# Performance work log

Hardware: AMD Instinct MI355X
Metric: run time of the kernel (lower is better)

## Reference

```python
import jax, jax.numpy as jnp
import numpy as np

B, N, M, D, H = 4, 1024, 1024, 1024, 16
HD = D // H
MH = int(D * 4.0 * 2 / 3)  # SwiGLU hidden = 2730
EPS = 1e-6


def setup_inputs() -> dict:
    key = jax.random.key(0)
    ks = jax.random.split(key, 16)
    w = lambda k, shape: jax.random.normal(k, shape, jnp.float32) * 0.02
    return dict(
        x=jax.random.normal(ks[0], (B, N, D), jnp.float32),
        source_tokens=jax.random.normal(ks[1], (B, M, D), jnp.float32),
        c=jax.random.normal(ks[2], (B, D), jnp.float32),
        ada_w=w(ks[3], (D, 9 * D)), ada_b=jnp.zeros((9 * D,), jnp.float32),
        n1_w=jnp.ones((D,), jnp.float32), nc_w=jnp.ones((D,), jnp.float32), n2_w=jnp.ones((D,), jnp.float32),
        sa_qkv_w=w(ks[4], (D, 3 * D)), sa_qkv_b=jnp.zeros((3 * D,), jnp.float32),
        sa_qn_w=jnp.ones((HD,), jnp.float32), sa_kn_w=jnp.ones((HD,), jnp.float32),
        sa_o_w=w(ks[5], (D, D)), sa_o_b=jnp.zeros((D,), jnp.float32),
        ca_q_w=w(ks[6], (D, D)), ca_q_b=jnp.zeros((D,), jnp.float32),
        ca_kv_w=w(ks[7], (D, 2 * D)), ca_kv_b=jnp.zeros((2 * D,), jnp.float32),
        ca_qn_w=jnp.ones((HD,), jnp.float32), ca_kn_w=jnp.ones((HD,), jnp.float32),
        ca_o_w=w(ks[8], (D, D)), ca_o_b=jnp.zeros((D,), jnp.float32),
        mlp_w1=w(ks[9], (D, MH)), mlp_b1=jnp.zeros((MH,), jnp.float32),
        mlp_w2=w(ks[10], (D, MH)), mlp_b2=jnp.zeros((MH,), jnp.float32),
        mlp_w3=w(ks[11], (MH, D)), mlp_b3=jnp.zeros((D,), jnp.float32),
    )


def _rms(x, w):
    return x * jax.lax.rsqrt(jnp.mean(x * x, axis=-1, keepdims=True) + EPS) * w


def _modulate(x, shift, scale):
    return x * (1.0 + scale[:, None, :]) + shift[:, None, :]


def _sdpa(q, k, v):
    # q: (B,Nq,H,HD), k/v: (B,Nk,H,HD)
    s = jnp.einsum('bqhd,bkhd->bhqk', q, k) * (HD ** -0.5)
    a = jax.nn.softmax(s, axis=-1)
    o = jnp.einsum('bhqk,bkhd->bqhd', a, v)
    return o.reshape(q.shape[0], q.shape[1], D)


def reference(x, source_tokens, c, ada_w, ada_b, n1_w, nc_w, n2_w,
              sa_qkv_w, sa_qkv_b, sa_qn_w, sa_kn_w, sa_o_w, sa_o_b,
              ca_q_w, ca_q_b, ca_kv_w, ca_kv_b, ca_qn_w, ca_kn_w, ca_o_w, ca_o_b,
              mlp_w1, mlp_b1, mlp_w2, mlp_b2, mlp_w3, mlp_b3):
    mods = jax.nn.silu(c) @ ada_w + ada_b
    (shift_sa, scale_sa, gate_sa, shift_ca, scale_ca, gate_ca,
     shift_ff, scale_ff, gate_ff) = jnp.split(mods, 9, axis=-1)

    # --- self-attention sublayer ---
    xn = _modulate(_rms(x, n1_w), shift_sa, scale_sa)
    qkv = xn @ sa_qkv_w + sa_qkv_b
    q, k, v = jnp.split(qkv, 3, axis=-1)
    q = _rms(q.reshape(B, N, H, HD), sa_qn_w)
    k = _rms(k.reshape(B, N, H, HD), sa_kn_w)
    v = v.reshape(B, N, H, HD)
    attn = _sdpa(q, k, v) @ sa_o_w + sa_o_b
    x = x + gate_sa[:, None, :] * attn

    # --- cross-attention sublayer ---
    xn = _modulate(_rms(x, nc_w), shift_ca, scale_ca)
    q = (xn @ ca_q_w + ca_q_b).reshape(B, N, H, HD)
    kv = source_tokens @ ca_kv_w + ca_kv_b
    k, v = jnp.split(kv, 2, axis=-1)
    q = _rms(q, ca_qn_w)
    k = _rms(k.reshape(B, M, H, HD), ca_kn_w)
    v = v.reshape(B, M, H, HD)
    cattn = _sdpa(q, k, v) @ ca_o_w + ca_o_b
    x = x + gate_ca[:, None, :] * cattn

    # --- SwiGLU FFN sublayer ---
    xn = _modulate(_rms(x, n2_w), shift_ff, scale_ff)
    ff = (jax.nn.silu(xn @ mlp_w1 + mlp_b1) * (xn @ mlp_w2 + mlp_b2)) @ mlp_w3 + mlp_b3
    x = x + gate_ff[:, None, :] * ff
    return x
```

## Files before the change

kernel.cpp:

```cpp
#include <hip/hip_runtime.h>

typedef unsigned short u16;
typedef __attribute__((ext_vector_type(8))) short short8;
typedef __attribute__((ext_vector_type(4))) float f32x4;

#define DD 1024
#define NN 1024
#define MODS_LD 9216

__device__ __forceinline__ float bf2f(u16 v) {
  unsigned int u = ((unsigned int)v) << 16;
  return __builtin_bit_cast(float, u);
}
__device__ __forceinline__ u16 f2bf(float f) {
  unsigned int u = __builtin_bit_cast(unsigned int, f);
  unsigned int lsb = (u >> 16) & 1;
  u += 0x7fffu + lsb;
  return (u16)(u >> 16);
}
__device__ __forceinline__ unsigned cvtpk_bf16(float a, float b) {
  unsigned r;
  asm volatile("v_cvt_pk_bf16_f32 %0, %1, %2" : "=v"(r) : "v"(a), "v"(b));
  return r;
}

__device__ __forceinline__ void gload_lds16(const u16* g, u16* l) {
  __builtin_amdgcn_global_load_lds(
      (const __attribute__((address_space(1))) unsigned int*)g,
      (__attribute__((address_space(3))) unsigned int*)l, 16, 0, 0);
}

__device__ __forceinline__ void xcd_tile(int ncolChunks, int cr, int cc, int& tm, int& tn) {
  int id = blockIdx.x;
  int c = id & 7, i = id >> 3;
  int chunkRow = c / ncolChunks, chunkCol = c % ncolChunks;
  tm = chunkRow * cr + (i % cr);
  tn = chunkCol * cc + (i / cr);
}

__global__ void transpose_convert(const float* __restrict__ src, u16* __restrict__ dst,
                                  int R, int C, int R2, int C2) {
  __shared__ float tile[32][33];
  int tx = threadIdx.x, ty = threadIdx.y;
  int r0 = blockIdx.x * 32, c0 = blockIdx.y * 32;
#pragma unroll
  for (int i = 0; i < 4; ++i) {
    int r = r0 + ty + i * 8, c = c0 + tx;
    tile[ty + i * 8][tx] = (r < R && c < C) ? src[(long)r * C + c] : 0.f;
  }
  __syncthreads();
#pragma unroll
  for (int i = 0; i < 4; ++i) {
    int c = c0 + ty + i * 8, r = r0 + tx;
    if (c < C2 && r < R2) dst[(long)c * R2 + r] = f2bf(tile[tx][ty + i * 8]);
  }
}

__global__ void cvt_bf16_kernel(const float* __restrict__ in, u16* __restrict__ out, long n4) {
  long i = (long)blockIdx.x * 256 + threadIdx.x;
  if (i >= n4) return;
  float4 v = *(const float4*)&in[i * 4];
  ushort4 pk = {f2bf(v.x), f2bf(v.y), f2bf(v.z), f2bf(v.w)};
  *(ushort4*)&out[i * 4] = pk;
}

__global__ void silu_kernel(const float* __restrict__ c, float* __restrict__ sc) {
  int i = blockIdx.x * 256 + threadIdx.x;
  float v = c[i];
  sc[i] = v / (1.f + __expf(-v));
}

#define MODS_KS 32
__global__ __launch_bounds__(256) void mods_partial(const float* __restrict__ sc,
                                                    const float* __restrict__ aw,
                                                    float* __restrict__ part) {
  int j = blockIdx.x * 256 + threadIdx.x;
  int ks = blockIdx.y;
  int d0 = ks * (DD / MODS_KS);
  float a0 = 0.f, a1 = 0.f, a2 = 0.f, a3 = 0.f;
#pragma unroll 8
  for (int d = d0; d < d0 + DD / MODS_KS; ++d) {
    float w = aw[(long)d * MODS_LD + j];
    a0 = fmaf(sc[d], w, a0);
    a1 = fmaf(sc[DD + d], w, a1);
    a2 = fmaf(sc[2 * DD + d], w, a2);
    a3 = fmaf(sc[3 * DD + d], w, a3);
  }
  long base = (long)ks * 4 * MODS_LD + j;
  part[base] = a0;
  part[base + MODS_LD] = a1;
  part[base + 2 * MODS_LD] = a2;
  part[base + 3 * MODS_LD] = a3;
}

__global__ __launch_bounds__(256) void mods_reduce(const float* __restrict__ part,
                                                   const float* __restrict__ ab,
                                                   float* __restrict__ mods) {
  int j = blockIdx.x * 256 + threadIdx.x;
  int b = blockIdx.y;
  float acc = ab[j];
#pragma unroll
  for (int ks = 0; ks < MODS_KS; ++ks) acc += part[((long)ks * 4 + b) * MODS_LD + j];
  mods[(long)b * MODS_LD + j] = acc;
}

__global__ __launch_bounds__(256) void rmsmod_kernel(const float* __restrict__ x,
                                                     const float* __restrict__ w,
                                                     const float* __restrict__ mods,
                                                     int shiftOff, int scaleOff,
                                                     u16* __restrict__ out) {
  long row = blockIdx.x;
  int b = (int)(row >> 10);
  int t = threadIdx.x;
  const float* xr = x + row * DD;
  float4 v = *(const float4*)&xr[t * 4];
  float ss = v.x * v.x + v.y * v.y + v.z * v.z + v.w * v.w;
#pragma unroll
  for (int msk = 1; msk < 64; msk <<= 1) ss += __shfl_xor(ss, msk);
  __shared__ float red[4];
  if ((t & 63) == 0) red[t >> 6] = ss;
  __syncthreads();
  float tot = red[0] + red[1] + red[2] + red[3];
  float inv = rsqrtf(tot * (1.f / DD) + 1e-6f);
  const float* mrow = mods + (long)b * MODS_LD;
  float vv[4] = {v.x, v.y, v.z, v.w};
  u16 tmp[4];
#pragma unroll
  for (int j = 0; j < 4; ++j) {
    int c = t * 4 + j;
    float rr = vv[j] * inv * w[c] * (1.f + mrow[scaleOff + c]) + mrow[shiftOff + c];
    tmp[j] = f2bf(rr);
  }
  ushort4 pk = {tmp[0], tmp[1], tmp[2], tmp[3]};
  *(ushort4*)&out[row * DD + t * 4] = pk;
}

__global__ void vtrans_kernel(const u16* __restrict__ vb, int kvStride, int Mpb,
                              u16* __restrict__ vt) {
  __shared__ u16 tile[64][66];
  int t = threadIdx.x;
  int kt = blockIdx.x, h = blockIdx.y, b = blockIdx.z;
  const u16* base = vb + ((long)(b * Mpb + kt * 64)) * kvStride + h * 64;
#pragma unroll
  for (int sh = 0; sh < 2; ++sh) {
    int r = sh * 32 + (t >> 3);
    int c0 = (t & 7) * 8;
    short8 vv = *(const short8*)(base + (long)r * kvStride + c0);
#pragma unroll
    for (int j = 0; j < 8; ++j) tile[c0 + j][r] = (u16)vv[j];
  }
  __syncthreads();
  u16* obase = vt + ((long)(b * 16 + h) * 64) * 1024 + kt * 64;
#pragma unroll
  for (int sh = 0; sh < 2; ++sh) {
    int d = sh * 32 + (t >> 3);
    int c0 = (t & 7) * 8;
    u16 tmp[8];
#pragma unroll
    for (int j = 0; j < 8; ++j) tmp[j] = tile[d][c0 + j];
    *(short8*)(obase + (long)d * 1024 + c0) = *(short8*)tmp;
  }
}

template <int MODE, int BN, int MINW, int NORM>
__global__ __launch_bounds__(256, MINW) void gemm_bf16(
    const u16* __restrict__ A, const u16* __restrict__ Bt, int K, int ldc,
    const float* __restrict__ bias, int biasN, u16* __restrict__ outb,
    float* __restrict__ outf, const float* __restrict__ xin,
    const float* __restrict__ mods, int gateOff, int ncolChunks, int cr, int cc,
    const float* __restrict__ nw, int normLo, int normHi, float nscale) {
  constexpr int WC = BN / 2;
  constexpr int NT = WC / 16;
  constexpr int LOADS = 4 + BN / 32;
  __shared__ u16 As[2][128 * 64];
  __shared__ u16 Bs[2][BN * 64];
  int t = threadIdx.x;
  int l = t & 63, w = t >> 6;
  int wr = w >> 1, wc = w & 1;
  int lg = l >> 4, ll = l & 15;
  int rx = ll & 7;
  int tm, tn;
  xcd_tile(ncolChunks, cr, cc, tm, tn);
  long rowTile = (long)tm * 128;
  long colTile = (long)tn * BN;
  const u16* Ap = A + rowTile * K;
  const u16* Bp = Bt + colTile * K;
  int srow = t >> 3;
  int sck = ((t & 7) ^ (srow & 7)) * 8;

  auto stage = [&](int buf, int k0) {
#pragma unroll
    for (int i = 0; i < 4; ++i)
      gload_lds16(Ap + (long)(i * 32 + srow) * K + k0 + sck, &As[buf][(i * 256 + t) * 8]);
#pragma unroll
    for (int i = 0; i < BN / 32; ++i)
      gload_lds16(Bp + (long)(i * 32 + srow) * K + k0 + sck, &Bs[buf][(i * 256 + t) * 8]);
  };

  const int ntk = K >> 6;
  stage(0, 0);
  if (ntk > 1) stage(1, 64);

  f32x4 acc[4][NT] = {};
  int cur = 0;
  for (int i = 0; i < ntk; ++i) {
    if (i + 1 < ntk) {
      asm volatile("s_waitcnt vmcnt(%0)" ::"i"(LOADS) : "memory");
    } else {
      asm volatile("s_waitcnt vmcnt(0)" ::: "memory");
    }
    __builtin_amdgcn_s_barrier();
    const u16* Ac = As[cur];
    const u16* Bc = Bs[cur];
    short8 af[2][4], bfr[2][NT];
#pragma unroll
    for (int kk = 0; kk < 2; ++kk) {
#pragma unroll
      for (int m2 = 0; m2 < 4; ++m2)
        af[kk][m2] =
            *(const short8*)&Ac[(wr * 64 + m2 * 16 + ll) * 64 + (((kk * 4 + lg) ^ rx) << 3)];
#pragma unroll
      for (int n2 = 0; n2 < NT; ++n2)
        bfr[kk][n2] =
            *(const short8*)&Bc[(wc * WC + n2 * 16 + ll) * 64 + (((kk * 4 + lg) ^ rx) << 3)];
    }
    asm volatile("s_waitcnt lgkmcnt(0)" ::: "memory");
    __builtin_amdgcn_sched_barrier(0);
    __builtin_amdgcn_s_barrier();
    if (i + 2 < ntk) stage(cur, (i + 2) * 64);
    __builtin_amdgcn_s_setprio(1);
#pragma unroll
    for (int kk = 0; kk < 2; ++kk)
#pragma unroll
      for (int m2 = 0; m2 < 4; ++m2)
#pragma unroll
        for (int n2 = 0; n2 < NT; ++n2)
          acc[m2][n2] = __builtin_amdgcn_mfma_f32_16x16x32_bf16(af[kk][m2], bfr[kk][n2],
                                                                acc[m2][n2], 0, 0, 0);
    __builtin_amdgcn_s_setprio(0);
    cur ^= 1;
  }

  if (NORM == 1 && tn >= normLo && tn < normHi) {
    float bv[NT], wnv[NT];
#pragma unroll
    for (int n2 = 0; n2 < NT; ++n2) {
      long cg = colTile + wc * WC + n2 * 16 + ll;
      bv[n2] = bias[cg];
      wnv[n2] = nw[n2 * 16 + ll];
    }
#pragma unroll
    for (int m2 = 0; m2 < 4; ++m2) {
#pragma unroll
      for (int r = 0; r < 4; ++r) {
        float vals[NT];
        float ss = 0.f;
#pragma unroll
        for (int n2 = 0; n2 < NT; ++n2) {
          vals[n2] = acc[m2][n2][r] + bv[n2];
          ss += vals[n2] * vals[n2];
        }
        ss += __shfl_xor(ss, 1);
        ss += __shfl_xor(ss, 2);
        ss += __shfl_xor(ss, 4);
        ss += __shfl_xor(ss, 8);
        float inv = rsqrtf(ss * (1.f / 64) + 1e-6f) * nscale;
        long rg = rowTile + wr * 64 + m2 * 16 + lg * 4 + r;
#pragma unroll
        for (int n2 = 0; n2 < NT; ++n2) {
          long cg = colTile + wc * WC + n2 * 16 + ll;
          outb[rg * ldc + cg] = f2bf(vals[n2] * inv * wnv[n2]);
        }
      }
    }
    return;
  }

#pragma unroll
  for (int n2 = 0; n2 < NT; ++n2) {
    long cg = colTile + wc * WC + n2 * 16 + ll;
    float bv = (cg < biasN) ? bias[cg] : 0.f;
#pragma unroll
    for (int m2 = 0; m2 < 4; ++m2) {
#pragma unroll
      for (int r = 0; r < 4; ++r) {
        long rg = rowTile + wr * 64 + m2 * 16 + lg * 4 + r;
        float v = acc[m2][n2][r] + bv;
        long idx = rg * ldc + cg;
        if (MODE == 0) {
          outb[idx] = f2bf(v);
        } else {
          int bb = (int)(rg >> 10);
          outf[idx] = xin[idx] + mods[(long)bb * MODS_LD + gateOff + cg] * v;
        }
      }
    }
  }
}

__global__ __launch_bounds__(256, 2) void gemm_dual_swiglu(
    const u16* __restrict__ A, const u16* __restrict__ B1t, const u16* __restrict__ B2t,
    int K, int ldc, const float* __restrict__ b1, const float* __restrict__ b2, int biasN,
    u16* __restrict__ outb, int ncolChunks, int cr, int cc) {
  constexpr int BN = 64, WC = 32, NT = 2;
  __shared__ u16 As[2][128 * 64];
  __shared__ u16 B1s[2][BN * 64];
  __shared__ u16 B2s[2][BN * 64];
  int t = threadIdx.x;
  int l = t & 63, w = t >> 6;
  int wr = w >> 1, wc = w & 1;
  int lg = l >> 4, ll = l & 15;
  int rx = ll & 7;
  int tm, tn;
  xcd_tile(ncolChunks, cr, cc, tm, tn);
  long rowTile = (long)tm * 128;
  long colTile = (long)tn * BN;
  const u16* Ap = A + rowTile * K;
  const u16* B1p = B1t + colTile * K;
  const u16* B2p = B2t + colTile * K;
  int srow = t >> 3;
  int sck = ((t & 7) ^ (srow & 7)) * 8;

  auto stage = [&](int buf, int k0) {
#pragma unroll
    for (int i = 0; i < 4; ++i)
      gload_lds16(Ap + (long)(i * 32 + srow) * K + k0 + sck, &As[buf][(i * 256 + t) * 8]);
#pragma unroll
    for (int i = 0; i < 2; ++i) {
      gload_lds16(B1p + (long)(i * 32 + srow) * K + k0 + sck, &B1s[buf][(i * 256 + t) * 8]);
      gload_lds16(B2p + (long)(i * 32 + srow) * K + k0 + sck, &B2s[buf][(i * 256 + t) * 8]);
    }
  };

  const int ntk = K >> 6;
  stage(0, 0);
  if (ntk > 1) stage(1, 64);

  f32x4 acc1[4][NT] = {}, acc2[4][NT] = {};
  int cur = 0;
  for (int i = 0; i < ntk; ++i) {
    if (i + 1 < ntk) {
      asm volatile("s_waitcnt vmcnt(8)" ::: "memory");
    } else {
      asm volatile("s_waitcnt vmcnt(0)" ::: "memory");
    }
    __builtin_amdgcn_s_barrier();
    const u16* Ac = As[cur];
    const u16* B1c = B1s[cur];
    const u16* B2c = B2s[cur];
    short8 af[2][4], b1f[2][NT], b2f[2][NT];
#pragma unroll
    for (int kk = 0; kk < 2; ++kk) {
#pragma unroll
      for (int m2 = 0; m2 < 4; ++m2)
        af[kk][m2] =
            *(const short8*)&Ac[(wr * 64 + m2 * 16 + ll) * 64 + (((kk * 4 + lg) ^ rx) << 3)];
#pragma unroll
      for (int n2 = 0; n2 < NT; ++n2) {
        int off = (wc * WC + n2 * 16 + ll) * 64 + (((kk * 4 + lg) ^ rx) << 3);
        b1f[kk][n2] = *(const short8*)&B1c[off];
        b2f[kk][n2] = *(const short8*)&B2c[off];
      }
    }
    asm volatile("s_waitcnt lgkmcnt(0)" ::: "memory");
    __builtin_amdgcn_sched_barrier(0);
    __builtin_amdgcn_s_barrier();
    if (i + 2 < ntk) stage(cur, (i + 2) * 64);
    __builtin_amdgcn_s_setprio(1);
#pragma unroll
    for (int kk = 0; kk < 2; ++kk)
#pragma unroll
      for (int m2 = 0; m2 < 4; ++m2)
#pragma unroll
        for (int n2 = 0; n2 < NT; ++n2) {
          acc1[m2][n2] = __builtin_amdgcn_mfma_f32_16x16x32_bf16(af[kk][m2], b1f[kk][n2],
                                                                 acc1[m2][n2], 0, 0, 0);
          acc2[m2][n2] = __builtin_amdgcn_mfma_f32_16x16x32_bf16(af[kk][m2], b2f[kk][n2],
                                                                 acc2[m2][n2], 0, 0, 0);
        }
    __builtin_amdgcn_s_setprio(0);
    cur ^= 1;
  }
#pragma unroll
  for (int n2 = 0; n2 < NT; ++n2) {
    long cg = colTile + wc * WC + n2 * 16 + ll;
    float bv1 = (cg < biasN) ? b1[cg] : 0.f;
    float bv2 = (cg < biasN) ? b2[cg] : 0.f;
#pragma unroll
    for (int m2 = 0; m2 < 4; ++m2) {
#pragma unroll
      for (int r = 0; r < 4; ++r) {
        long rg = rowTile + wr * 64 + m2 * 16 + lg * 4 + r;
        float v1 = acc1[m2][n2][r] + bv1;
        float v2 = acc2[m2][n2][r] + bv2;
        float sg = v1 / (1.f + __expf(-v1));
        outb[rg * ldc + cg] = f2bf(sg * v2);
      }
    }
  }
}

__global__ __launch_bounds__(256, 3) void attn_kernel(
    const u16* __restrict__ qb, int qStride, const u16* __restrict__ kb, int kvStride,
    const u16* __restrict__ vt, const float* __restrict__ qn, u16* __restrict__ outp,
    int Nk, int Mpb) {
  __shared__ u16 Qs[64 * 64];
  __shared__ u16 Ks[2][64 * 64];
  __shared__ u16 Vs[2][64 * 64];
  __shared__ u16 Ps[4][16 * 64];
  int t = threadIdx.x, w = t >> 6, l = t & 63;
  int h = blockIdx.x, b = blockIdx.y, qt = blockIdx.z;
  int lg = l >> 4, ll = l & 15;
  int rx = ll & 7;

  const u16* Qbase = qb + ((long)(b * NN + qt * 64)) * qStride + h * 64;
  const u16* Kbase = kb + ((long)b * Mpb) * kvStride + h * 64;
  const u16* Vbase = vt + ((long)(b * 16 + h) * 64) * 1024;

  int srow = t >> 3;
  int schunk = t & 7;

#pragma unroll
  for (int sh = 0; sh < 2; ++sh) {
    int row = sh * 32 + srow;
    int ck = schunk ^ (row & 7);
    gload_lds16(Qbase + (long)row * qStride + ck * 8, &Qs[sh * 2048 + t * 8]);
  }
  auto stageKV = [&](int buf, int kt) {
    const u16* kn = Kbase + (long)kt * 64 * kvStride;
    const u16* vn = Vbase + kt * 64;
#pragma unroll
    for (int sh = 0; sh < 2; ++sh) {
      int row = sh * 32 + srow;
      int ck = schunk ^ (row & 7);
      gload_lds16(kn + (long)row * kvStride + ck * 8, &Ks[buf][sh * 2048 + t * 8]);
      gload_lds16(vn + (long)row * 1024 + ck * 8, &Vs[buf][sh * 2048 + t * 8]);
    }
  };
  const int ntk = Nk >> 6;
  stageKV(0, 0);
  if (ntk > 1) stageKV(1, 1);

  short8 qf0, qf1;
  float mrun = -1e30f, ssum = 0.f;
  f32x4 o[4] = {};

  int cur = 0;
  for (int kt = 0; kt < ntk; ++kt) {
    if (kt + 1 < ntk) {
      asm volatile("s_waitcnt vmcnt(4)" ::: "memory");
    } else {
      asm volatile("s_waitcnt vmcnt(0)" ::: "memory");
    }
    __builtin_amdgcn_s_barrier();
    if (kt == 0) {
      qf0 = *(const short8*)&Qs[(w * 16 + ll) * 64 + ((lg ^ rx) << 3)];
      qf1 = *(const short8*)&Qs[(w * 16 + ll) * 64 + (((4 + lg) ^ rx) << 3)];
      float qv0[8], qv1[8], ss = 0.f;
#pragma unroll
      for (int j = 0; j < 8; ++j) {
        qv0[j] = bf2f((u16)qf0[j]);
        qv1[j] = bf2f((u16)qf1[j]);
        ss += qv0[j] * qv0[j] + qv1[j] * qv1[j];
      }
      ss += __shfl_xor(ss, 16);
      ss += __shfl_xor(ss, 32);
      float inv = rsqrtf(ss * (1.f / 64) + 1e-6f) * 0.125f;
      int d0 = (lg ^ rx) << 3, d1 = ((4 + lg) ^ rx) << 3;
      u16 t0[8], t1[8];
#pragma unroll
      for (int j = 0; j < 8; ++j) {
        t0[j] = f2bf(qv0[j] * inv * qn[d0 + j]);
        t1[j] = f2bf(qv1[j] * inv * qn[d1 + j]);
      }
      qf0 = *(short8*)t0;
      qf1 = *(short8*)t1;
    }
    const u16* Kc = Ks[cur];
    f32x4 s[4] = {};
#pragma unroll
    for (int n = 0; n < 4; ++n) {
      short8 kf0 = *(const short8*)&Kc[(n * 16 + ll) * 64 + ((lg ^ rx) << 3)];
      short8 kf1 = *(const short8*)&Kc[(n * 16 + ll) * 64 + (((4 + lg) ^ rx) << 3)];
      s[n] = __builtin_amdgcn_mfma_f32_16x16x32_bf16(kf0, qf0, s[n], 0, 0, 0);
      s[n] = __builtin_amdgcn_mfma_f32_16x16x32_bf16(kf1, qf1, s[n], 0, 0, 0);
    }
    float t0 = fmaxf(fmaxf(s[0][0], s[0][1]), fmaxf(s[0][2], s[0][3]));
    float t1 = fmaxf(fmaxf(s[1][0], s[1][1]), fmaxf(s[1][2], s[1][3]));
    float t2 = fmaxf(fmaxf(s[2][0], s[2][1]), fmaxf(s[2][2], s[2][3]));
    float t3 = fmaxf(fmaxf(s[3][0], s[3][1]), fmaxf(s[3][2], s[3][3]));
    float pm = fmaxf(fmaxf(t0, t1), fmaxf(t2, t3));
    pm = fmaxf(pm, __shfl_xor(pm, 16));
    pm = fmaxf(pm, __shfl_xor(pm, 32));
    float nm = fmaxf(mrun, pm);
    float alpha = __expf(mrun - nm);
    float pn[4][4];
#pragma unroll
    for (int n = 0; n < 4; ++n)
#pragma unroll
      for (int r = 0; r < 4; ++r) pn[n][r] = __expf(s[n][r] - nm);
    float r0 = (pn[0][0] + pn[0][1]) + (pn[0][2] + pn[0][3]);
    float r1 = (pn[1][0] + pn[1][1]) + (pn[1][2] + pn[1][3]);
    float r2 = (pn[2][0] + pn[2][1]) + (pn[2][2] + pn[2][3]);
    float r3 = (pn[3][0] + pn[3][1]) + (pn[3][2] + pn[3][3]);
    float rs = (r0 + r1) + (r2 + r3);
    rs += __shfl_xor(rs, 16);
    rs += __shfl_xor(rs, 32);
    ssum = ssum * alpha + rs;
    mrun = nm;
#pragma unroll
    for (int n = 0; n < 4; ++n) {
      uint2 pkd;
      pkd.x = cvtpk_bf16(pn[n][0], pn[n][1]);
      pkd.y = cvtpk_bf16(pn[n][2], pn[n][3]);
      int gran = n * 2 + (lg >> 1);
      int perm = gran ^ rx;
      *(uint2*)&Ps[w][ll * 64 + perm * 8 + (lg & 1) * 4] = pkd;
    }
    float a0 = __shfl(alpha, lg * 4 + 0);
    float a1 = __shfl(alpha, lg * 4 + 1);
    float a2 = __shfl(alpha, lg * 4 + 2);
    float a3 = __shfl(alpha, lg * 4 + 3);
#pragma unroll
    for (int n = 0; n < 4; ++n) {
      o[n][0] *= a0;
      o[n][1] *= a1;
      o[n][2] *= a2;
      o[n][3] *= a3;
    }
    short8 pf0 = *(const short8*)&Ps[w][ll * 64 + ((lg ^ rx) << 3)];
    short8 pf1 = *(const short8*)&Ps[w][ll * 64 + (((4 + lg) ^ rx) << 3)];
    const u16* Vc = Vs[cur];
    short8 vfr[4][2];
#pragma unroll
    for (int n = 0; n < 4; ++n) {
      vfr[n][0] = *(const short8*)&Vc[(n * 16 + ll) * 64 + ((lg ^ rx) << 3)];
      vfr[n][1] = *(const short8*)&Vc[(n * 16 + ll) * 64 + (((4 + lg) ^ rx) << 3)];
    }
    asm volatile("s_waitcnt lgkmcnt(0)" ::: "memory");
    __builtin_amdgcn_sched_barrier(0);
    __builtin_amdgcn_s_barrier();
    if (kt + 2 < ntk) stageKV(cur, kt + 2);
    __builtin_amdgcn_s_setprio(1);
#pragma unroll
    for (int n = 0; n < 4; ++n) {
      o[n] = __builtin_amdgcn_mfma_f32_16x16x32_bf16(pf0, vfr[n][0], o[n], 0, 0, 0);
      o[n] = __builtin_amdgcn_mfma_f32_16x16x32_bf16(pf1, vfr[n][1], o[n], 0, 0, 0);
    }
    __builtin_amdgcn_s_setprio(0);
    cur ^= 1;
  }
  float s0 = __shfl(ssum, lg * 4 + 0);
  float s1 = __shfl(ssum, lg * 4 + 1);
  float s2 = __shfl(ssum, lg * 4 + 2);
  float s3 = __shfl(ssum, lg * 4 + 3);
  float i0 = 1.f / s0, i1 = 1.f / s1, i2 = 1.f / s2, i3 = 1.f / s3;
#pragma unroll
  for (int n = 0; n < 4; ++n) {
    float ir[4] = {i0, i1, i2, i3};
#pragma unroll
    for (int r = 0; r < 4; ++r) {
      long row = (long)b * NN + qt * 64 + w * 16 + lg * 4 + r;
      int col = h * 64 + n * 16 + ll;
      outp[row * DD + col] = f2bf(o[n][r] * ir[r]);
    }
  }
}

extern "C" void kernel_launch(void* const* d_in, const int* in_sizes, int n_in,
                              void* d_out, int out_size, void* d_ws, size_t ws_size,
                              hipStream_t stream) {
  const float* x = (const float*)d_in[0];
  const float* src = (const float*)d_in[1];
  const float* c = (const float*)d_in[2];
  const float* ada_w = (const float*)d_in[3];
  const float* ada_b = (const float*)d_in[4];
  const float* n1_w = (const float*)d_in[5];
  const float* nc_w = (const float*)d_in[6];
  const float* n2_w = (const float*)d_in[7];
  const float* sa_qkv_w = (const float*)d_in[8];
  const float* sa_qkv_b = (const float*)d_in[9];
  const float* sa_qn_w = (const float*)d_in[10];
  const float* sa_kn_w = (const float*)d_in[11];
  const float* sa_o_w = (const float*)d_in[12];
  const float* sa_o_b = (const float*)d_in[13];
  const float* ca_q_w = (const float*)d_in[14];
  const float* ca_q_b = (const float*)d_in[15];
  const float* ca_kv_w = (const float*)d_in[16];
  const float* ca_kv_b = (const float*)d_in[17];
  const float* ca_qn_w = (const float*)d_in[18];
  const float* ca_kn_w = (const float*)d_in[19];
  const float* ca_o_w = (const float*)d_in[20];
  const float* ca_o_b = (const float*)d_in[21];
  const float* mlp_w1 = (const float*)d_in[22];
  const float* mlp_b1 = (const float*)d_in[23];
  const float* mlp_w2 = (const float*)d_in[24];
  const float* mlp_b2 = (const float*)d_in[25];
  const float* mlp_w3 = (const float*)d_in[26];
  const float* mlp_b3 = (const float*)d_in[27];
  float* out = (float*)d_out;

  char* p = (char*)d_ws;
  auto alloc = [&](size_t bytes) {
    char* r = p;
    p += (bytes + 255) & ~(size_t)255;
    return r;
  };
  float* mods = (float*)alloc(4l * 9216 * 4);
  float* sc = (float*)alloc(4096l * 4);
  float* part = (float*)alloc((long)MODS_KS * 4 * 9216 * 4);
  u16* qkvT = (u16*)alloc(3072l * 1024 * 2);
  u16* saoT = (u16*)alloc(1024l * 1024 * 2);
  u16* caqT = (u16*)alloc(1024l * 1024 * 2);
  u16* cakvT = (u16*)alloc(2048l * 1024 * 2);
  u16* caoT = (u16*)alloc(1024l * 1024 * 2);
  u16* w1T = (u16*)alloc(2816l * 1024 * 2);
  u16* w2T = (u16*)alloc(2816l * 1024 * 2);
  u16* w3T = (u16*)alloc(1024l * 2816 * 2);
  u16* xnb = (u16*)alloc(4096l * 1024 * 2);
  u16* srcb = (u16*)alloc(4096l * 1024 * 2);
  u16* bufA = (u16*)alloc(4096l * 3072 * 2);
  u16* bufB = (u16*)alloc(4096l * 2816 * 2);
  u16* attO = (u16*)alloc(4096l * 1024 * 2);
  u16* vtb = xnb;

  dim3 tb(32, 8);
  transpose_convert<<<dim3(32, 96), tb, 0, stream>>>(sa_qkv_w, qkvT, 1024, 3072, 1024, 3072);
  transpose_convert<<<dim3(32, 32), tb, 0, stream>>>(sa_o_w, saoT, 1024, 1024, 1024, 1024);
  transpose_convert<<<dim3(32, 32), tb, 0, stream>>>(ca_q_w, caqT, 1024, 1024, 1024, 1024);
  transpose_convert<<<dim3(32, 64), tb, 0, stream>>>(ca_kv_w, cakvT, 1024, 2048, 1024, 2048);
  transpose_convert<<<dim3(32, 32), tb, 0, stream>>>(ca_o_w, caoT, 1024, 1024, 1024, 1024);
  transpose_convert<<<dim3(32, 88), tb, 0, stream>>>(mlp_w1, w1T, 1024, 2730, 1024, 2816);
  transpose_convert<<<dim3(32, 88), tb, 0, stream>>>(mlp_w2, w2T, 1024, 2730, 1024, 2816);
  transpose_convert<<<dim3(88, 32), tb, 0, stream>>>(mlp_w3, w3T, 2730, 1024, 2816, 1024);
  cvt_bf16_kernel<<<4096, 256, 0, stream>>>(src, srcb, 4096l * 1024 / 4);
  silu_kernel<<<16, 256, 0, stream>>>(c, sc);
  mods_partial<<<dim3(36, MODS_KS), 256, 0, stream>>>(sc, ada_w, part);
  mods_reduce<<<dim3(36, 4), 256, 0, stream>>>(part, ada_b, mods);

  rmsmod_kernel<<<4096, 256, 0, stream>>>(x, n1_w, mods, 0, 1024, xnb);
  gemm_bf16<0, 128, 2, 1><<<768, 256, 0, stream>>>(xnb, qkvT, 1024, 3072, sa_qkv_b, 3072, bufA,
                                                   nullptr, nullptr, nullptr, 0, 4, 16, 6,
                                                   sa_kn_w, 8, 16, 1.0f);
  vtrans_kernel<<<dim3(16, 16, 4), 256, 0, stream>>>(bufA + 2048, 3072, 1024, vtb);
  attn_kernel<<<dim3(16, 4, 16), 256, 0, stream>>>(bufA, 3072, bufA + 1024, 3072, vtb, sa_qn_w,
                                                   attO, 1024, 1024);
  gemm_bf16<1, 64, 3, 0><<<512, 256, 0, stream>>>(attO, saoT, 1024, 1024, sa_o_b, 1024, nullptr,
                                                  out, x, mods, 2048, 2, 8, 8, nullptr, 0, 0,
                                                  0.f);

  rmsmod_kernel<<<4096, 256, 0, stream>>>(out, nc_w, mods, 3072, 4096, xnb);
  gemm_bf16<0, 64, 3, 0><<<512, 256, 0, stream>>>(xnb, caqT, 1024, 1024, ca_q_b, 1024, bufA,
                                                  nullptr, nullptr, nullptr, 0, 2, 8, 8,
                                                  nullptr, 0, 0, 0.f);
  gemm_bf16<0, 128, 2, 1><<<512, 256, 0, stream>>>(srcb, cakvT, 1024, 2048, ca_kv_b, 2048, bufB,
                                                   nullptr, nullptr, nullptr, 0, 2, 8, 8,
                                                   ca_kn_w, 0, 8, 1.0f);
  vtrans_kernel<<<dim3(16, 16, 4), 256, 0, stream>>>(bufB + 1024, 2048, 1024, vtb);
  attn_kernel<<<dim3(16, 4, 16), 256, 0, stream>>>(bufA, 1024, bufB, 2048, vtb, ca_qn_w, attO,
                                                   1024, 1024);
  gemm_bf16<1, 64, 3, 0><<<512, 256, 0, stream>>>(attO, caoT, 1024, 1024, ca_o_b, 1024, nullptr,
                                                  out, out, mods, 5120, 2, 8, 8, nullptr, 0, 0,
                                                  0.f);

  rmsmod_kernel<<<4096, 256, 0, stream>>>(out, n2_w, mods, 6144, 7168, xnb);
  gemm_dual_swiglu<<<1408, 256, 0, stream>>>(xnb, w1T, w2T, 1024, 2816, mlp_b1, mlp_b2, 2730,
                                             bufA, 4, 16, 11);
  gemm_bf16<1, 64, 3, 0><<<512, 256, 0, stream>>>(bufA, w3T, 2816, 1024, mlp_b3, 1024, nullptr,
                                                  out, out, mods, 8192, 2, 8, 8, nullptr, 0, 0,
                                                  0.f);
}
```

Measured before the change: 372.2 us.

## Batch weight transposes, fuse SiLU into mods, use lazy-rescale exp2 softmax

Eight separate weight transpose launches become one launch that reads a table of descriptors. The SiLU kernel is folded into mods_partial through a small shared-memory staging step. The attention softmax now works in base 2: log2(e) is folded into the Q scale and v_exp_f32 is called directly. The running max is only updated, and the output only rescaled, when the new block max exceeds the old one by more than 8, which cuts exp and multiply work per tile at the cost of a small added overflow and precision risk.

Measured after the change: 362.3 us. 2.7% less time.

```diff
diff --git a/kernel.cpp b/kernel.cpp
--- a/kernel.cpp
+++ b/kernel.cpp
@@ -21,6 +21,11 @@
 __device__ __forceinline__ unsigned cvtpk_bf16(float a, float b) {
   unsigned r;
   asm volatile("v_cvt_pk_bf16_f32 %0, %1, %2" : "=v"(r) : "v"(a), "v"(b));
+  return r;
+}
+__device__ __forceinline__ float exp2x(float x) {
+  float r;
+  asm("v_exp_f32 %0, %1" : "=v"(r) : "v"(x));
   return r;
 }
 
@@ -38,11 +43,29 @@
   tn = chunkCol * cc + (i / cr);
 }
 
-__global__ void transpose_convert(const float* __restrict__ src, u16* __restrict__ dst,
-                                  int R, int C, int R2, int C2) {
+struct TDesc {
+  const float* s;
+  u16* d;
+  int R, C, R2, C2, gx, start;
+};
+struct TPack {
+  TDesc t[8];
+};
+
+__global__ void transpose_all(TPack p) {
   __shared__ float tile[32][33];
+  int id = blockIdx.x;
+  int k = 0;
+#pragma unroll
+  for (int j = 1; j < 8; ++j)
+    if (id >= p.t[j].start) k = j;
+  const float* src = p.t[k].s;
+  u16* dst = p.t[k].d;
+  int R = p.t[k].R, C = p.t[k].C, R2 = p.t[k].R2, C2 = p.t[k].C2;
+  int rem = id - p.t[k].start;
+  int gx = p.t[k].gx;
+  int r0 = (rem % gx) * 32, c0 = (rem / gx) * 32;
   int tx = threadIdx.x, ty = threadIdx.y;
-  int r0 = blockIdx.x * 32, c0 = blockIdx.y * 32;
 #pragma unroll
   for (int i = 0; i < 4; ++i) {
     int r = r0 + ty + i * 8, c = c0 + tx;
@@ -64,27 +87,31 @@
   *(ushort4*)&out[i * 4] = pk;
 }
 
-__global__ void silu_kernel(const float* __restrict__ c, float* __restrict__ sc) {
-  int i = blockIdx.x * 256 + threadIdx.x;
-  float v = c[i];
-  sc[i] = v / (1.f + __expf(-v));
-}
-
 #define MODS_KS 32
-__global__ __launch_bounds__(256) void mods_partial(const float* __restrict__ sc,
+__global__ __launch_bounds__(256) void mods_partial(const float* __restrict__ c,
                                                     const float* __restrict__ aw,
                                                     float* __restrict__ part) {
+  __shared__ float scs[4][32];
   int j = blockIdx.x * 256 + threadIdx.x;
   int ks = blockIdx.y;
   int d0 = ks * (DD / MODS_KS);
+  int t = threadIdx.x;
+  if (t < 32) {
+#pragma unroll
+    for (int b2 = 0; b2 < 4; ++b2) {
+      float v = c[b2 * DD + d0 + t];
+      scs[b2][t] = v / (1.f + __expf(-v));
+    }
+  }
+  __syncthreads();
   float a0 = 0.f, a1 = 0.f, a2 = 0.f, a3 = 0.f;
 #pragma unroll 8
-  for (int d = d0; d < d0 + DD / MODS_KS; ++d) {
-    float w = aw[(long)d * MODS_LD + j];
-    a0 = fmaf(sc[d], w, a0);
-    a1 = fmaf(sc[DD + d], w, a1);
-    a2 = fmaf(sc[2 * DD + d], w, a2);
-    a3 = fmaf(sc[3 * DD + d], w, a3);
+  for (int d = 0; d < DD / MODS_KS; ++d) {
+    float w = aw[(long)(d0 + d) * MODS_LD + j];
+    a0 = fmaf(scs[0][d], w, a0);
+    a1 = fmaf(scs[1][d], w, a1);
+    a2 = fmaf(scs[2][d], w, a2);
+    a3 = fmaf(scs[3][d], w, a3);
   }
   long base = (long)ks * 4 * MODS_LD + j;
   part[base] = a0;
@@ -465,7 +492,7 @@
       }
       ss += __shfl_xor(ss, 16);
       ss += __shfl_xor(ss, 32);
-      float inv = rsqrtf(ss * (1.f / 64) + 1e-6f) * 0.125f;
+      float inv = rsqrtf(ss * (1.f / 64) + 1e-6f) * (0.125f * 1.44269504f);
       int d0 = (lg ^ rx) << 3, d1 = ((4 + lg) ^ rx) << 3;
       u16 t0[8], t1[8];
 #pragma unroll
@@ -492,13 +519,13 @@
     float pm = fmaxf(fmaxf(t0, t1), fmaxf(t2, t3));
     pm = fmaxf(pm, __shfl_xor(pm, 16));
     pm = fmaxf(pm, __shfl_xor(pm, 32));
-    float nm = fmaxf(mrun, pm);
-    float alpha = __expf(mrun - nm);
+    bool resc = !__all(pm - mrun <= 8.f);
+    float nm = resc ? fmaxf(mrun, pm) : mrun;
     float pn[4][4];
 #pragma unroll
     for (int n = 0; n < 4; ++n)
 #pragma unroll
-      for (int r = 0; r < 4; ++r) pn[n][r] = __expf(s[n][r] - nm);
+      for (int r = 0; r < 4; ++r) pn[n][r] = exp2x(s[n][r] - nm);
     float r0 = (pn[0][0] + pn[0][1]) + (pn[0][2] + pn[0][3]);
     float r1 = (pn[1][0] + pn[1][1]) + (pn[1][2] + pn[1][3]);
     float r2 = (pn[2][0] + pn[2][1]) + (pn[2][2] + pn[2][3]);
@@ -506,7 +533,23 @@
     float rs = (r0 + r1) + (r2 + r3);
     rs += __shfl_xor(rs, 16);
     rs += __shfl_xor(rs, 32);
-    ssum = ssum * alpha + rs;
+    if (resc) {
+      float alpha = exp2x(mrun - nm);
+      ssum = ssum * alpha + rs;
+      float a0 = __shfl(alpha, lg * 4 + 0);
+      float a1 = __shfl(alpha, lg * 4 + 1);
+      float a2 = __shfl(alpha, lg * 4 + 2);
+      float a3 = __shfl(alpha, lg * 4 + 3);
+#pragma unroll
+      for (int n = 0; n < 4; ++n) {
+        o[n][0] *= a0;
+        o[n][1] *= a1;
+        o[n][2] *= a2;
+        o[n][3] *= a3;
+      }
+    } else {
+      ssum += rs;
+    }
     mrun = nm;
 #pragma unroll
     for (int n = 0; n < 4; ++n) {
@@ -516,17 +559,6 @@
       int gran = n * 2 + (lg >> 1);
       int perm = gran ^ rx;
       *(uint2*)&Ps[w][ll * 64 + perm * 8 + (lg & 1) * 4] = pkd;
-    }
-    float a0 = __shfl(alpha, lg * 4 + 0);
-    float a1 = __shfl(alpha, lg * 4 + 1);
-    float a2 = __shfl(alpha, lg * 4 + 2);
-    float a3 = __shfl(alpha, lg * 4 + 3);
-#pragma unroll
-    for (int n = 0; n < 4; ++n) {
-      o[n][0] *= a0;
-      o[n][1] *= a1;
-      o[n][2] *= a2;
-      o[n][3] *= a3;
     }
     short8 pf0 = *(const short8*)&Ps[w][ll * 64 + ((lg ^ rx) << 3)];
     short8 pf1 = *(const short8*)&Ps[w][ll * 64 + (((4 + lg) ^ rx) << 3)];
@@ -607,7 +639,6 @@
     return r;
   };
   float* mods = (float*)alloc(4l * 9216 * 4);
-  float* sc = (float*)alloc(4096l * 4);
   float* part = (float*)alloc((long)MODS_KS * 4 * 9216 * 4);
   u16* qkvT = (u16*)alloc(3072l * 1024 * 2);
   u16* saoT = (u16*)alloc(1024l * 1024 * 2);
@@ -624,18 +655,18 @@
   u16* attO = (u16*)alloc(4096l * 1024 * 2);
   u16* vtb = xnb;
 
-  dim3 tb(32, 8);
-  transpose_convert<<<dim3(32, 96), tb, 0, stream>>>(sa_qkv_w, qkvT, 1024, 3072, 1024, 3072);
-  transpose_convert<<<dim3(32, 32), tb, 0, stream>>>(sa_o_w, saoT, 1024, 1024, 1024, 1024);
-  transpose_convert<<<dim3(32, 32), tb, 0, stream>>>(ca_q_w, caqT, 1024, 1024, 1024, 1024);
-  transpose_convert<<<dim3(32, 64), tb, 0, stream>>>(ca_kv_w, cakvT, 1024, 2048, 1024, 2048);
-  transpose_convert<<<dim3(32, 32), tb, 0, stream>>>(ca_o_w, caoT, 1024, 1024, 1024, 1024);
-  transpose_convert<<<dim3(32, 88), tb, 0, stream>>>(mlp_w1, w1T, 1024, 2730, 1024, 2816);
-  transpose_convert<<<dim3(32, 88), tb, 0, stream>>>(mlp_w2, w2T, 1024, 2730, 1024, 2816);
-  transpose_convert<<<dim3(88, 32), tb, 0, stream>>>(mlp_w3, w3T, 2730, 1024, 2816, 1024);
+  TPack tp;
+  tp.t[0] = {sa_qkv_w, qkvT, 1024, 3072, 1024, 3072, 32, 0};
+  tp.t[1] = {sa_o_w, saoT, 1024, 1024, 1024, 1024, 32, 3072};
+  tp.t[2] = {ca_q_w, caqT, 1024, 1024, 1024, 1024, 32, 4096};
+  tp.t[3] = {ca_kv_w, cakvT, 1024, 2048, 1024, 2048, 32, 5120};
+  tp.t[4] = {ca_o_w, caoT, 1024, 1024, 1024, 1024, 32, 7168};
+  tp.t[5] = {mlp_w1, w1T, 1024, 2730, 1024, 2816, 32, 8192};
+  tp.t[6] = {mlp_w2, w2T, 1024, 2730, 1024, 2816, 32, 11008};
+  tp.t[7] = {mlp_w3, w3T, 2730, 1024, 2816, 1024, 88, 13824};
+  transpose_all<<<16640, dim3(32, 8), 0, stream>>>(tp);
   cvt_bf16_kernel<<<4096, 256, 0, stream>>>(src, srcb, 4096l * 1024 / 4);
-  silu_kernel<<<16, 256, 0, stream>>>(c, sc);
-  mods_partial<<<dim3(36, MODS_KS), 256, 0, stream>>>(sc, ada_w, part);
+  mods_partial<<<dim3(36, MODS_KS), 256, 0, stream>>>(c, ada_w, part);
   mods_reduce<<<dim3(36, 4), 256, 0, stream>>>(part, ada_b, mods);
 
   rmsmod_kernel<<<4096, 256, 0, stream>>>(x, n1_w, mods, 0, 1024, xnb);
```
